# Performance work log

Hardware: AMD Instinct MI355X
Metric: run time of the kernel (lower is better)

## Reference

```python
import jax, jax.numpy as jnp
import numpy as np

B, C, H, W = 4, 256, 64, 64

def _conv1x1(x, w, b):
    # x: [B,C,H,W], w: [O,C] (1x1 conv kernel squeezed), b: [O]
    return jnp.einsum('bchw,oc->bohw', x, w) + b[None, :, None, None]

def setup_inputs() -> dict:
    key = jax.random.key(0)
    ks = jax.random.split(key, 9)
    s = 1.0 / np.sqrt(C)
    inp = {'x': jax.random.normal(ks[0], (B, C, H, W), dtype=jnp.float32)}
    for i, name in enumerate(['f', 'g', 'h', 'v']):
        inp['W' + name] = jax.random.uniform(ks[1 + 2 * i], (C, C), jnp.float32, -s, s)
        inp['b' + name] = jax.random.uniform(ks[2 + 2 * i], (C,), jnp.float32, -s, s)
    return inp

def reference(x, Wf, bf, Wg, bg, Wh, bh, Wv, bv):
    b, c, h, w = x.shape
    n = h * w
    f = _conv1x1(x, Wf, bf).reshape(b, c, n)  # [B,C,N]
    g = _conv1x1(x, Wg, bg).reshape(b, c, n)  # [B,C,N]
    hh = _conv1x1(x, Wh, bh).reshape(b, c, n)  # [B,C,N]
    fg = jnp.einsum('bci,bcj->bij', f, g)      # [B,N,N], no scaling (as in source)
    attn = jax.nn.softmax(fg, axis=1)          # softmax over dim=1 (first N axis)
    fgh = jnp.einsum('bci,bij->bcj', hh, attn) # [B,C,N]
    return _conv1x1(fgh.reshape(b, c, h, w), Wv, bv)
```

## Files before the change

kernel.cpp:

```cpp
#include <hip/hip_runtime.h>
#include <hip/hip_bf16.h>


typedef short short8 __attribute__((ext_vector_type(8)));
typedef float f32x4 __attribute__((ext_vector_type(4)));
typedef _Float16 f16x8 __attribute__((ext_vector_type(8)));
typedef unsigned short u16;

#define DEV static __device__ __forceinline__
#define MFMA(a, b, c)   __builtin_amdgcn_mfma_f32_16x16x32_bf16(a, b, c, 0, 0, 0)
#define MFMA16(a, b, c) __builtin_amdgcn_mfma_f32_16x16x32_f16(a, b, c, 0, 0, 0)

DEV u16 b16(float x) {
    __hip_bfloat16 h = __float2bfloat16(x);
    return *reinterpret_cast<u16*>(&h);
}
DEV float f16f(u16 u) {
    union { unsigned int ui; float f; } c;
    c.ui = ((unsigned int)u) << 16;
    return c.f;
}
DEV u16 h16(float x) {
    union { _Float16 h; u16 u; } c;
    c.h = (_Float16)x;
    return c.u;
}
DEV short8 ld8(const u16* p) { return *reinterpret_cast<const short8*>(p); }
DEV f16x8 ldh8(const u16* p) { return *reinterpret_cast<const f16x8*>(p); }

DEV void gload16(const void* g, void* l) {
    __builtin_amdgcn_global_load_lds(
        (const __attribute__((address_space(1))) unsigned int*)g,
        (__attribute__((address_space(3))) unsigned int*)l, 16, 0, 0);
}

constexpr size_t OFF_WFH = 0;
constexpr size_t OFF_WFL = 131072;
constexpr size_t OFF_WGH = 262144;
constexpr size_t OFF_WGL = 393216;
constexpr size_t OFF_WHB = 524288;
constexpr size_t OFF_WVB = 655360;
constexpr size_t OFF_ML  = 786432;
constexpr size_t OFF_F   = 1310720;
constexpr size_t OFF_G   = OFF_F + 8388608;
constexpr size_t OFF_H   = OFF_G + 8388608;
constexpr size_t OFF_XTH = OFF_H + 8388608;
constexpr size_t OFF_XTL = OFF_XTH + 8388608;
constexpr size_t OFF_OP  = OFF_XTH;
constexpr size_t OFF_OT  = OFF_F;

__global__ __launch_bounds__(256) void k_prep_w(
    const float* __restrict__ Wf, const float* __restrict__ Wg,
    const float* __restrict__ Wh, const float* __restrict__ Wv,
    u16* WFH, u16* WFL, u16* WGH, u16* WGL, u16* WHB, u16* WVB) {
    int i = blockIdx.x * 256 + threadIdx.x;
    float fv = Wf[i];
    u16 fh = b16(fv);
    WFH[i] = fh;
    WFL[i] = b16(fv - f16f(fh));
    float gv = Wg[i];
    u16 gh = b16(gv);
    WGH[i] = gh;
    WGL[i] = b16(gv - f16f(gh));
    WHB[i] = b16(Wh[i]);
    WVB[i] = h16(Wv[i]);
}

__global__ __launch_bounds__(256) void k_prep_x(const float* __restrict__ x, u16* XtH, u16* XtL) {
    __shared__ float lds[64][65];
    int bid = blockIdx.x;
    int b = bid >> 8, rem = bid & 255, ct = rem >> 6, nt = rem & 63;
    int tid = threadIdx.x;
    int tx = tid & 63, ty = tid >> 6;
    const float* src = x + ((size_t)(b * 256 + ct * 64)) * 4096 + nt * 64;
#pragma unroll
    for (int k = 0; k < 16; ++k) {
        int cl = ty * 16 + k;
        lds[cl][tx] = src[(size_t)cl * 4096 + tx];
    }
    __syncthreads();
    int nl = tid >> 2, cg = tid & 3;
    short8 h0, h1, l0, l1;
#pragma unroll
    for (int j = 0; j < 8; ++j) {
        float v = lds[cg * 16 + j][nl];
        u16 hb = b16(v);
        h0[j] = (short)hb;
        l0[j] = (short)b16(v - f16f(hb));
    }
#pragma unroll
    for (int j = 8; j < 16; ++j) {
        float v = lds[cg * 16 + j][nl];
        u16 hb = b16(v);
        h1[j - 8] = (short)hb;
        l1[j - 8] = (short)b16(v - f16f(hb));
    }
    size_t dst = ((size_t)(b * 4096 + nt * 64 + nl)) * 256 + ct * 64 + cg * 16;
    *reinterpret_cast<short8*>(XtH + dst) = h0;
    *reinterpret_cast<short8*>(XtH + dst + 8) = h1;
    *reinterpret_cast<short8*>(XtL + dst) = l0;
    *reinterpret_cast<short8*>(XtL + dst + 8) = l1;
}

__global__ __launch_bounds__(256) void k_conv_fg(
    const u16* __restrict__ XtH, const u16* __restrict__ XtL,
    const u16* __restrict__ WFH, const u16* __restrict__ WFL,
    const u16* __restrict__ WGH, const u16* __restrict__ WGL,
    const float* __restrict__ bf, const float* __restrict__ bg,
    u16* F, u16* G) {
    int bidm = blockIdx.x & 255, bido = blockIdx.x >> 8;
    int w = threadIdx.x >> 6, lane = threadIdx.x & 63, r = lane & 15, g = lane >> 4;
    int m0 = bidm * 64 + w * 16, o0 = bido * 64;
    f32x4 fa[4], ga[4];
#pragma unroll
    for (int i = 0; i < 4; ++i) { fa[i] = {0.f, 0.f, 0.f, 0.f}; ga[i] = {0.f, 0.f, 0.f, 0.f}; }
    const u16* arh = XtH + (size_t)(m0 + r) * 256;
    const u16* arl = XtL + (size_t)(m0 + r) * 256;
#pragma unroll
    for (int ks = 0; ks < 8; ++ks) {
        int k0 = ks * 32 + 8 * g;
        short8 ah = ld8(arh + k0);
        short8 al = ld8(arl + k0);
#pragma unroll
        for (int ot = 0; ot < 4; ++ot) {
            size_t wrow = (size_t)(o0 + ot * 16 + r) * 256 + k0;
            short8 wfh = ld8(WFH + wrow), wfl = ld8(WFL + wrow);
            short8 wgh = ld8(WGH + wrow), wgl = ld8(WGL + wrow);
            fa[ot] = MFMA(ah, wfh, fa[ot]);
            fa[ot] = MFMA(ah, wfl, fa[ot]);
            fa[ot] = MFMA(al, wfh, fa[ot]);
            ga[ot] = MFMA(ah, wgh, ga[ot]);
            ga[ot] = MFMA(ah, wgl, ga[ot]);
            ga[ot] = MFMA(al, wgh, ga[ot]);
        }
    }
#pragma unroll
    for (int ot = 0; ot < 4; ++ot) {
#pragma unroll
        for (int q = 0; q < 4; ++q) {
            int row = m0 + 4 * g + q;
            int col = o0 + ot * 16 + r;
            size_t idx = (size_t)row * 256 + col;
            F[idx] = h16(fa[ot][q] + bf[col]);
            G[idx] = h16(ga[ot][q] + bg[col]);
        }
    }
}

__global__ __launch_bounds__(256) void k_conv_h(
    const u16* __restrict__ WHB, const u16* __restrict__ XtH,
    const float* __restrict__ bh, u16* Hb) {
    int bidn = blockIdx.x & 255, bido = blockIdx.x >> 8;
    int w = threadIdx.x >> 6, lane = threadIdx.x & 63, r = lane & 15, g = lane >> 4;
    int o0 = bido * 64 + w * 16, n0 = bidn * 64;
    f32x4 acc[4];
#pragma unroll
    for (int i = 0; i < 4; ++i) acc[i] = {0.f, 0.f, 0.f, 0.f};
    const u16* arow = WHB + (size_t)(o0 + r) * 256;
#pragma unroll
    for (int ks = 0; ks < 8; ++ks) {
        int k0 = ks * 32 + 8 * g;
        short8 a = ld8(arow + k0);
#pragma unroll
        for (int ntl = 0; ntl < 4; ++ntl) {
            short8 bb = ld8(XtH + (size_t)(n0 + ntl * 16 + r) * 256 + k0);
            acc[ntl] = MFMA(a, bb, acc[ntl]);
        }
    }
#pragma unroll
    for (int ntl = 0; ntl < 4; ++ntl) {
#pragma unroll
        for (int q = 0; q < 4; ++q) {
            int o = o0 + 4 * g + q;
            int nf = n0 + ntl * 16 + r;
            int bb = nf >> 12, n = nf & 4095;
            Hb[((size_t)(bb * 256 + o)) * 4096 + n] = h16(acc[ntl][q] + bh[o]);
        }
    }
}

DEV float rmax16(float v) {
    v = fmaxf(v, __shfl_xor(v, 1));
    v = fmaxf(v, __shfl_xor(v, 2));
    v = fmaxf(v, __shfl_xor(v, 4));
    v = fmaxf(v, __shfl_xor(v, 8));
    return v;
}
DEV float rsum16(float v) {
    v += __shfl_xor(v, 1);
    v += __shfl_xor(v, 2);
    v += __shfl_xor(v, 4);
    v += __shfl_xor(v, 8);
    return v;
}

__global__ __launch_bounds__(256, 2) void k_attn(
    const u16* __restrict__ F, const u16* __restrict__ G,
    const u16* __restrict__ Hb, u16* __restrict__ OP, float* __restrict__ ML) {
    __shared__ u16 Klds[16384];
    __shared__ u16 Vlds[16384];

    int bid = blockIdx.x;
    int xcd = bid & 7;
    int b = xcd >> 1, ks = xcd & 1;
    int jt = bid >> 3;
    int tid = threadIdx.x;
    int w = tid >> 6, lane = tid & 63, r = lane & 15, g = lane >> 4;
    int j0 = jt * 64 + w * 16;
    const float L2E = 1.4426950408889634f;

    f16x8 Qf[8];
    {
        const u16* q = G + (size_t)(b * 4096 + j0 + r) * 256;
#pragma unroll
        for (int k = 0; k < 8; ++k) Qf[k] = ldh8(q + k * 32 + 8 * g);
    }
    f32x4 O[16];
#pragma unroll
    for (int i = 0; i < 16; ++i) O[i] = {0.f, 0.f, 0.f, 0.f};
    float m[4], l[4];
#pragma unroll
    for (int q = 0; q < 4; ++q) { m[q] = -1e30f; l[q] = 0.f; }

    const char* Fb  = (const char*)(F + (size_t)b * 4096 * 256);
    const char* Hbb = (const char*)(Hb + (size_t)b * 256 * 4096);
    char* Kl = (char*)Klds;
    char* Vl = (char*)Vlds;
    u16* Pw = Klds + w * 1280;

    for (int i0 = ks * 2048; i0 < ks * 2048 + 2048; i0 += 64) {
#pragma unroll
        for (int t = 0; t < 8; ++t) {
            int ti = w * 8 + t;
            int d = ti * 1024 + lane * 16;
            int row = d >> 9, cp = d & 511;
            gload16(Fb + (((size_t)(i0 + row)) << 9) + (size_t)(cp ^ ((row & 7) << 4)),
                    Kl + ti * 1024);
        }
#pragma unroll
        for (int t = 0; t < 8; ++t) {
            int ti = w * 8 + t;
            int d = ti * 1024 + lane * 16;
            int c = d >> 7, kb = d & 127;
            gload16(Hbb + (((size_t)c) << 13) + (size_t)(i0 * 2) + (size_t)(kb ^ ((c & 7) << 4)),
                    Vl + ti * 1024);
        }
        __syncthreads();

        f32x4 s[4];
#pragma unroll
        for (int it = 0; it < 4; ++it) s[it] = {0.f, 0.f, 0.f, 0.f};
#pragma unroll
        for (int it = 0; it < 4; ++it) {
            int row = it * 16 + r;
            const char* kr = Kl + row * 512;
            int sw = (row & 7) << 4;
#pragma unroll
            for (int k = 0; k < 8; ++k) {
                f16x8 kb = *reinterpret_cast<const f16x8*>(kr + ((k * 64 + 16 * g) ^ sw));
                s[it] = MFMA16(Qf[k], kb, s[it]);
            }
        }
        float corr[4];
#pragma unroll
        for (int q = 0; q < 4; ++q) {
            float v = fmaxf(fmaxf(s[0][q], s[1][q]), fmaxf(s[2][q], s[3][q]));
            v = rmax16(v);
            float mn = fmaxf(m[q], v);
            corr[q] = exp2f((m[q] - mn) * L2E);
            float rs = 0.f;
#pragma unroll
            for (int it = 0; it < 4; ++it) {
                float pv = exp2f((s[it][q] - mn) * L2E);
                s[it][q] = pv;
                rs += pv;
            }
            rs = rsum16(rs);
            l[q] = l[q] * corr[q] + rs;
            m[q] = mn;
        }
#pragma unroll
        for (int ct = 0; ct < 16; ++ct) {
            O[ct][0] *= corr[0];
            O[ct][1] *= corr[1];
            O[ct][2] *= corr[2];
            O[ct][3] *= corr[3];
        }
        __syncthreads();

#pragma unroll
        for (int it = 0; it < 4; ++it) {
#pragma unroll
            for (int q = 0; q < 4; ++q) Pw[(4 * g + q) * 72 + it * 16 + r] = h16(s[it][q]);
        }
        __asm__ volatile("s_waitcnt lgkmcnt(0)" ::: "memory");
        f16x8 pa0 = *reinterpret_cast<const f16x8*>((const char*)Pw + r * 144 + 16 * g);
        f16x8 pa1 = *reinterpret_cast<const f16x8*>((const char*)Pw + r * 144 + 64 + 16 * g);

#pragma unroll
        for (int ct = 0; ct < 16; ++ct) {
            int c = ct * 16 + r;
            const char* vr = Vl + c * 128;
            int sw = (c & 7) << 4;
            f16x8 v0 = *reinterpret_cast<const f16x8*>(vr + ((16 * g) ^ sw));
            f16x8 v1 = *reinterpret_cast<const f16x8*>(vr + ((64 + 16 * g) ^ sw));
            O[ct] = MFMA16(pa0, v0, O[ct]);
            O[ct] = MFMA16(pa1, v1, O[ct]);
        }
        __syncthreads();
    }
#pragma unroll
    for (int ct = 0; ct < 16; ++ct) {
#pragma unroll
        for (int q = 0; q < 4; ++q) {
            OP[((size_t)ks * 16384 + b * 4096 + j0 + 4 * g + q) * 256 + ct * 16 + r] = h16(O[ct][q]);
        }
    }
    if (r == 0) {
#pragma unroll
        for (int q = 0; q < 4; ++q) {
            size_t mi = ((size_t)ks * 16384 + b * 4096 + j0 + 4 * g + q) * 2;
            ML[mi] = m[q];
            ML[mi + 1] = l[q];
        }
    }
}

__global__ __launch_bounds__(256) void k_merge(
    const u16* __restrict__ OP, const float* __restrict__ ML, u16* __restrict__ OT) {
    int t = blockIdx.x * 256 + threadIdx.x;
    int m = t >> 5;
    int c0 = (t & 31) * 8;
    const float L2E = 1.4426950408889634f;
    float m0 = ML[(size_t)m * 2], l0 = ML[(size_t)m * 2 + 1];
    float m1 = ML[((size_t)16384 + m) * 2], l1 = ML[((size_t)16384 + m) * 2 + 1];
    float M = fmaxf(m0, m1);
    float w0 = exp2f((m0 - M) * L2E), w1 = exp2f((m1 - M) * L2E);
    float inv = 1.f / (w0 * l0 + w1 * l1);
    f16x8 v0 = ldh8(OP + (size_t)m * 256 + c0);
    f16x8 v1 = ldh8(OP + ((size_t)16384 + m) * 256 + c0);
    short8 outp;
#pragma unroll
    for (int j = 0; j < 8; ++j) outp[j] = (short)h16((w0 * (float)v0[j] + w1 * (float)v1[j]) * inv);
    *reinterpret_cast<short8*>(OT + (size_t)m * 256 + c0) = outp;
}

__global__ __launch_bounds__(256) void k_conv_out(
    const u16* __restrict__ WVB, const u16* __restrict__ OT,
    const float* __restrict__ bv, float* __restrict__ out) {
    int bidn = blockIdx.x & 255, bido = blockIdx.x >> 8;
    int w = threadIdx.x >> 6, lane = threadIdx.x & 63, r = lane & 15, g = lane >> 4;
    int o0 = bido * 64 + w * 16, n0 = bidn * 64;
    f32x4 acc[4];
#pragma unroll
    for (int i = 0; i < 4; ++i) acc[i] = {0.f, 0.f, 0.f, 0.f};
    const u16* arow = WVB + (size_t)(o0 + r) * 256;
#pragma unroll
    for (int ks = 0; ks < 8; ++ks) {
        int k0 = ks * 32 + 8 * g;
        f16x8 a = ldh8(arow + k0);
#pragma unroll
        for (int ntl = 0; ntl < 4; ++ntl) {
            f16x8 bb = ldh8(OT + (size_t)(n0 + ntl * 16 + r) * 256 + k0);
            acc[ntl] = MFMA16(a, bb, acc[ntl]);
        }
    }
#pragma unroll
    for (int ntl = 0; ntl < 4; ++ntl) {
#pragma unroll
        for (int q = 0; q < 4; ++q) {
            int o = o0 + 4 * g + q;
            int nf = n0 + ntl * 16 + r;
            int bb = nf >> 12, n = nf & 4095;
            out[((size_t)(bb * 256 + o)) * 4096 + n] = acc[ntl][q] + bv[o];
        }
    }
}

extern "C" void kernel_launch(void* const* d_in, const int* in_sizes, int n_in,
                              void* d_out, int out_size, void* d_ws, size_t ws_size,
                              hipStream_t stream) {
    const float* x  = (const float*)d_in[0];
    const float* Wf = (const float*)d_in[1];
    const float* bf = (const float*)d_in[2];
    const float* Wg = (const float*)d_in[3];
    const float* bg = (const float*)d_in[4];
    const float* Wh = (const float*)d_in[5];
    const float* bh = (const float*)d_in[6];
    const float* Wv = (const float*)d_in[7];
    const float* bv = (const float*)d_in[8];
    float* out = (float*)d_out;
    char* ws = (char*)d_ws;

    u16* WFH = (u16*)(ws + OFF_WFH);
    u16* WFL = (u16*)(ws + OFF_WFL);
    u16* WGH = (u16*)(ws + OFF_WGH);
    u16* WGL = (u16*)(ws + OFF_WGL);
    u16* WHB = (u16*)(ws + OFF_WHB);
    u16* WVB = (u16*)(ws + OFF_WVB);
    float* ML = (float*)(ws + OFF_ML);
    u16* F   = (u16*)(ws + OFF_F);
    u16* G   = (u16*)(ws + OFF_G);
    u16* H   = (u16*)(ws + OFF_H);
    u16* XTH = (u16*)(ws + OFF_XTH);
    u16* XTL = (u16*)(ws + OFF_XTL);
    u16* OP  = (u16*)(ws + OFF_OP);
    u16* OT  = (u16*)(ws + OFF_OT);

    k_prep_w<<<256, 256, 0, stream>>>(Wf, Wg, Wh, Wv, WFH, WFL, WGH, WGL, WHB, WVB);
    k_prep_x<<<1024, 256, 0, stream>>>(x, XTH, XTL);
    k_conv_fg<<<1024, 256, 0, stream>>>(XTH, XTL, WFH, WFL, WGH, WGL, bf, bg, F, G);
    k_conv_h<<<1024, 256, 0, stream>>>(WHB, XTH, bh, H);
    k_attn<<<512, 256, 0, stream>>>(F, G, H, OP, ML);
    k_merge<<<2048, 256, 0, stream>>>(OP, ML, OT);
    k_conv_out<<<1024, 256, 0, stream>>>(WVB, OT, bv, out);
}
```

Before: 254.9 us.

## Double-buffer attention K/V tiles, drop split-K merge, add lazy rescale

The attention kernel now walks all 4096 keys per block instead of splitting them across two blocks, which removes the partial-output/ML writes and the separate merge kernel. K and V tiles are double-buffered in LDS with global_load_lds prefetch of the next tile, and P gets its own LDS buffer, so one barrier per iteration replaces three. A lazy rescale skips the O correction when the running max grows by at most 8. The costs are half as many blocks (256), single-block occupancy from the larger LDS footprint, and a longer serial loop per block.

```diff
diff --git a/kernel.cpp b/kernel.cpp
--- a/kernel.cpp
+++ b/kernel.cpp
@@ -40,14 +40,12 @@
 constexpr size_t OFF_WGL = 393216;
 constexpr size_t OFF_WHB = 524288;
 constexpr size_t OFF_WVB = 655360;
-constexpr size_t OFF_ML  = 786432;
 constexpr size_t OFF_F   = 1310720;
 constexpr size_t OFF_G   = OFF_F + 8388608;
 constexpr size_t OFF_H   = OFF_G + 8388608;
 constexpr size_t OFF_XTH = OFF_H + 8388608;
 constexpr size_t OFF_XTL = OFF_XTH + 8388608;
-constexpr size_t OFF_OP  = OFF_XTH;
-constexpr size_t OFF_OT  = OFF_F;
+constexpr size_t OFF_OT  = OFF_XTH;
 
 __global__ __launch_bounds__(256) void k_prep_w(
     const float* __restrict__ Wf, const float* __restrict__ Wg,
@@ -194,19 +192,20 @@
     return v;
 }
 
-__global__ __launch_bounds__(256, 2) void k_attn(
+__global__ __launch_bounds__(256, 1) void k_attn(
     const u16* __restrict__ F, const u16* __restrict__ G,
-    const u16* __restrict__ Hb, u16* __restrict__ OP, float* __restrict__ ML) {
-    __shared__ u16 Klds[16384];
-    __shared__ u16 Vlds[16384];
+    const u16* __restrict__ Hb, u16* __restrict__ OT) {
+    __shared__ u16 Kd[2][16384];
+    __shared__ u16 Vd[2][16384];
+    __shared__ u16 Pd[4][1280];
 
     int bid = blockIdx.x;
     int xcd = bid & 7;
-    int b = xcd >> 1, ks = xcd & 1;
+    int b = xcd >> 1, half = xcd & 1;
     int jt = bid >> 3;
     int tid = threadIdx.x;
     int w = tid >> 6, lane = tid & 63, r = lane & 15, g = lane >> 4;
-    int j0 = jt * 64 + w * 16;
+    int j0 = half * 2048 + jt * 64 + w * 16;
     const float L2E = 1.4426950408889634f;
 
     f16x8 Qf[8];
@@ -224,74 +223,102 @@
 
     const char* Fb  = (const char*)(F + (size_t)b * 4096 * 256);
     const char* Hbb = (const char*)(Hb + (size_t)b * 256 * 4096);
-    char* Kl = (char*)Klds;
-    char* Vl = (char*)Vlds;
-    u16* Pw = Klds + w * 1280;
-
-    for (int i0 = ks * 2048; i0 < ks * 2048 + 2048; i0 += 64) {
-#pragma unroll
-        for (int t = 0; t < 8; ++t) {
-            int ti = w * 8 + t;
-            int d = ti * 1024 + lane * 16;
-            int row = d >> 9, cp = d & 511;
-            gload16(Fb + (((size_t)(i0 + row)) << 9) + (size_t)(cp ^ ((row & 7) << 4)),
-                    Kl + ti * 1024);
-        }
-#pragma unroll
-        for (int t = 0; t < 8; ++t) {
-            int ti = w * 8 + t;
-            int d = ti * 1024 + lane * 16;
-            int c = d >> 7, kb = d & 127;
-            gload16(Hbb + (((size_t)c) << 13) + (size_t)(i0 * 2) + (size_t)(kb ^ ((c & 7) << 4)),
-                    Vl + ti * 1024);
-        }
+    u16* Pw = Pd[w];
+
+    int koff[8], voff[8];
+#pragma unroll
+    for (int t = 0; t < 8; ++t) {
+        int d = (w * 8 + t) * 1024 + lane * 16;
+        koff[t] = d ^ (((d >> 9) & 7) << 4);
+        int c = d >> 7, kb = d & 127;
+        voff[t] = (c << 13) + (kb ^ (((c & 7)) << 4));
+    }
+
+#define STAGE(nxt, I0)                                                          \
+    do {                                                                        \
+        const char* kbase = Fb + (size_t)(I0) * 512;                            \
+        const char* vbase = Hbb + (size_t)(I0) * 2;                             \
+        char* kl = (char*)Kd[nxt];                                              \
+        char* vl = (char*)Vd[nxt];                                              \
+        _Pragma("unroll") for (int t = 0; t < 8; ++t)                           \
+            gload16(kbase + koff[t], kl + (w * 8 + t) * 1024);                  \
+        _Pragma("unroll") for (int t = 0; t < 8; ++t)                           \
+            gload16(vbase + voff[t], vl + (w * 8 + t) * 1024);                  \
+    } while (0)
+
+    STAGE(0, 0);
+
+    for (int it = 0; it < 64; ++it) {
+        int cur = it & 1;
         __syncthreads();
-
+        if (it + 1 < 64) STAGE(cur ^ 1, (it + 1) * 64);
+
+        const char* Kl = (const char*)Kd[cur];
+        const char* Vl = (const char*)Vd[cur];
         f32x4 s[4];
 #pragma unroll
-        for (int it = 0; it < 4; ++it) s[it] = {0.f, 0.f, 0.f, 0.f};
-#pragma unroll
-        for (int it = 0; it < 4; ++it) {
-            int row = it * 16 + r;
+        for (int it2 = 0; it2 < 4; ++it2) s[it2] = {0.f, 0.f, 0.f, 0.f};
+#pragma unroll
+        for (int it2 = 0; it2 < 4; ++it2) {
+            int row = it2 * 16 + r;
             const char* kr = Kl + row * 512;
             int sw = (row & 7) << 4;
 #pragma unroll
             for (int k = 0; k < 8; ++k) {
                 f16x8 kb = *reinterpret_cast<const f16x8*>(kr + ((k * 64 + 16 * g) ^ sw));
-                s[it] = MFMA16(Qf[k], kb, s[it]);
+                s[it2] = MFMA16(Qf[k], kb, s[it2]);
             }
         }
-        float corr[4];
+
+        float nm[4], grow = -1e30f;
 #pragma unroll
         for (int q = 0; q < 4; ++q) {
             float v = fmaxf(fmaxf(s[0][q], s[1][q]), fmaxf(s[2][q], s[3][q]));
             v = rmax16(v);
-            float mn = fmaxf(m[q], v);
-            corr[q] = exp2f((m[q] - mn) * L2E);
-            float rs = 0.f;
-#pragma unroll
-            for (int it = 0; it < 4; ++it) {
-                float pv = exp2f((s[it][q] - mn) * L2E);
-                s[it][q] = pv;
-                rs += pv;
+            nm[q] = v;
+            grow = fmaxf(grow, v - m[q]);
+        }
+        if (__all(grow <= 8.0f)) {
+#pragma unroll
+            for (int q = 0; q < 4; ++q) {
+                float rs = 0.f;
+#pragma unroll
+                for (int it2 = 0; it2 < 4; ++it2) {
+                    float pv = exp2f((s[it2][q] - m[q]) * L2E);
+                    s[it2][q] = pv;
+                    rs += pv;
+                }
+                l[q] += rsum16(rs);
             }
-            rs = rsum16(rs);
-            l[q] = l[q] * corr[q] + rs;
-            m[q] = mn;
-        }
-#pragma unroll
-        for (int ct = 0; ct < 16; ++ct) {
-            O[ct][0] *= corr[0];
-            O[ct][1] *= corr[1];
-            O[ct][2] *= corr[2];
-            O[ct][3] *= corr[3];
-        }
-        __syncthreads();
-
-#pragma unroll
-        for (int it = 0; it < 4; ++it) {
-#pragma unroll
-            for (int q = 0; q < 4; ++q) Pw[(4 * g + q) * 72 + it * 16 + r] = h16(s[it][q]);
+        } else {
+            float corr[4];
+#pragma unroll
+            for (int q = 0; q < 4; ++q) {
+                float mn = fmaxf(m[q], nm[q]);
+                corr[q] = exp2f((m[q] - mn) * L2E);
+                float rs = 0.f;
+#pragma unroll
+                for (int it2 = 0; it2 < 4; ++it2) {
+                    float pv = exp2f((s[it2][q] - mn) * L2E);
+                    s[it2][q] = pv;
+                    rs += pv;
+                }
+                l[q] = l[q] * corr[q] + rsum16(rs);
+                m[q] = mn;
+            }
+#pragma unroll
+            for (int ct = 0; ct < 16; ++ct) {
+                O[ct][0] *= corr[0];
+                O[ct][1] *= corr[1];
+                O[ct][2] *= corr[2];
+                O[ct][3] *= corr[3];
+            }
+        }
+
+#pragma unroll
+        for (int it2 = 0; it2 < 4; ++it2) {
+#pragma unroll
+            for (int q = 0; q < 4; ++q) Pw[(4 * g + q) * 72 + it2 * 16 + r] = h16(s[it2][q]);
         }
         __asm__ volatile("s_waitcnt lgkmcnt(0)" ::: "memory");
         f16x8 pa0 = *reinterpret_cast<const f16x8*>((const char*)Pw + r * 144 + 16 * g);
@@ -307,42 +334,19 @@
             O[ct] = MFMA16(pa0, v0, O[ct]);
             O[ct] = MFMA16(pa1, v1, O[ct]);
         }
-        __syncthreads();
-    }
+    }
+#undef STAGE
+
+    float inv[4];
+#pragma unroll
+    for (int q = 0; q < 4; ++q) inv[q] = 1.f / l[q];
 #pragma unroll
     for (int ct = 0; ct < 16; ++ct) {
 #pragma unroll
         for (int q = 0; q < 4; ++q) {
-            OP[((size_t)ks * 16384 + b * 4096 + j0 + 4 * g + q) * 256 + ct * 16 + r] = h16(O[ct][q]);
-        }
-    }
-    if (r == 0) {
-#pragma unroll
-        for (int q = 0; q < 4; ++q) {
-            size_t mi = ((size_t)ks * 16384 + b * 4096 + j0 + 4 * g + q) * 2;
-            ML[mi] = m[q];
-            ML[mi + 1] = l[q];
-        }
-    }
-}
-
-__global__ __launch_bounds__(256) void k_merge(
-    const u16* __restrict__ OP, const float* __restrict__ ML, u16* __restrict__ OT) {
-    int t = blockIdx.x * 256 + threadIdx.x;
-    int m = t >> 5;
-    int c0 = (t & 31) * 8;
-    const float L2E = 1.4426950408889634f;
-    float m0 = ML[(size_t)m * 2], l0 = ML[(size_t)m * 2 + 1];
-    float m1 = ML[((size_t)16384 + m) * 2], l1 = ML[((size_t)16384 + m) * 2 + 1];
-    float M = fmaxf(m0, m1);
-    float w0 = exp2f((m0 - M) * L2E), w1 = exp2f((m1 - M) * L2E);
-    float inv = 1.f / (w0 * l0 + w1 * l1);
-    f16x8 v0 = ldh8(OP + (size_t)m * 256 + c0);
-    f16x8 v1 = ldh8(OP + ((size_t)16384 + m) * 256 + c0);
-    short8 outp;
-#pragma unroll
-    for (int j = 0; j < 8; ++j) outp[j] = (short)h16((w0 * (float)v0[j] + w1 * (float)v1[j]) * inv);
-    *reinterpret_cast<short8*>(OT + (size_t)m * 256 + c0) = outp;
+            OT[(size_t)(b * 4096 + j0 + 4 * g + q) * 256 + ct * 16 + r] = h16(O[ct][q] * inv[q]);
+        }
+    }
 }
 
 __global__ __launch_bounds__(256) void k_conv_out(
@@ -398,20 +402,17 @@
     u16* WGL = (u16*)(ws + OFF_WGL);
     u16* WHB = (u16*)(ws + OFF_WHB);
     u16* WVB = (u16*)(ws + OFF_WVB);
-    float* ML = (float*)(ws + OFF_ML);
     u16* F   = (u16*)(ws + OFF_F);
     u16* G   = (u16*)(ws + OFF_G);
     u16* H   = (u16*)(ws + OFF_H);
     u16* XTH = (u16*)(ws + OFF_XTH);
     u16* XTL = (u16*)(ws + OFF_XTL);
-    u16* OP  = (u16*)(ws + OFF_OP);
     u16* OT  = (u16*)(ws + OFF_OT);
 
     k_prep_w<<<256, 256, 0, stream>>>(Wf, Wg, Wh, Wv, WFH, WFL, WGH, WGL, WHB, WVB);
     k_prep_x<<<1024, 256, 0, stream>>>(x, XTH, XTL);
     k_conv_fg<<<1024, 256, 0, stream>>>(XTH, XTL, WFH, WFL, WGH, WGL, bf, bg, F, G);
     k_conv_h<<<1024, 256, 0, stream>>>(WHB, XTH, bh, H);
-    k_attn<<<512, 256, 0, stream>>>(F, G, H, OP, ML);
-    k_merge<<<2048, 256, 0, stream>>>(OP, ML, OT);
+    k_attn<<<256, 256, 0, stream>>>(F, G, H, OT);
     k_conv_out<<<1024, 256, 0, stream>>>(WVB, OT, bv, out);
 }
```

After: 305.3 us. +19.8%, slower.

## Double-buffer K/V tiles in attention with lazy softmax rescaling and prio hints

Applied to the files above, without the earlier changes.

The attention kernel now double-buffers 32-key K and V tiles in shared memory, issuing the next tile's loads before computing on the current one. This is meant to hide global-load latency and removes one barrier per iteration. It also skips the running-max update and accumulator rescale when the max grows by at most 8, raises wave priority around MFMA blocks, and normalizes partial outputs before the merge. The cost is twice as many loop iterations on smaller tiles, and the lazy max risks fp16 overflow of the exp terms if the threshold is too loose.

```diff
diff --git a/kernel.cpp b/kernel.cpp
--- a/kernel.cpp
+++ b/kernel.cpp
@@ -6,6 +6,7 @@
 typedef float f32x4 __attribute__((ext_vector_type(4)));
 typedef _Float16 f16x8 __attribute__((ext_vector_type(8)));
 typedef unsigned short u16;
+typedef unsigned int u32;
 
 #define DEV static __device__ __forceinline__
 #define MFMA(a, b, c)   __builtin_amdgcn_mfma_f32_16x16x32_bf16(a, b, c, 0, 0, 0)
@@ -197,16 +198,16 @@
 __global__ __launch_bounds__(256, 2) void k_attn(
     const u16* __restrict__ F, const u16* __restrict__ G,
     const u16* __restrict__ Hb, u16* __restrict__ OP, float* __restrict__ ML) {
-    __shared__ u16 Klds[16384];
-    __shared__ u16 Vlds[16384];
+    __shared__ u16 Kd[2][8192];
+    __shared__ u16 Vd[2][8192];
+    __shared__ u16 Pd[4][1152];
 
     int bid = blockIdx.x;
-    int xcd = bid & 7;
+    int xcd = bid & 7, idx = bid >> 3;
     int b = xcd >> 1, ks = xcd & 1;
-    int jt = bid >> 3;
     int tid = threadIdx.x;
     int w = tid >> 6, lane = tid & 63, r = lane & 15, g = lane >> 4;
-    int j0 = jt * 64 + w * 16;
+    int j0 = idx * 64 + w * 16;
     const float L2E = 1.4426950408889634f;
 
     f16x8 Qf[8];
@@ -224,96 +225,131 @@
 
     const char* Fb  = (const char*)(F + (size_t)b * 4096 * 256);
     const char* Hbb = (const char*)(Hb + (size_t)b * 256 * 4096);
-    char* Kl = (char*)Klds;
-    char* Vl = (char*)Vlds;
-    u16* Pw = Klds + w * 1280;
-
-    for (int i0 = ks * 2048; i0 < ks * 2048 + 2048; i0 += 64) {
-#pragma unroll
-        for (int t = 0; t < 8; ++t) {
-            int ti = w * 8 + t;
-            int d = ti * 1024 + lane * 16;
-            int row = d >> 9, cp = d & 511;
-            gload16(Fb + (((size_t)(i0 + row)) << 9) + (size_t)(cp ^ ((row & 7) << 4)),
-                    Kl + ti * 1024);
-        }
-#pragma unroll
-        for (int t = 0; t < 8; ++t) {
-            int ti = w * 8 + t;
-            int d = ti * 1024 + lane * 16;
-            int c = d >> 7, kb = d & 127;
-            gload16(Hbb + (((size_t)c) << 13) + (size_t)(i0 * 2) + (size_t)(kb ^ ((c & 7) << 4)),
-                    Vl + ti * 1024);
-        }
-        __syncthreads();
-
-        f32x4 s[4];
-#pragma unroll
-        for (int it = 0; it < 4; ++it) s[it] = {0.f, 0.f, 0.f, 0.f};
-#pragma unroll
-        for (int it = 0; it < 4; ++it) {
-            int row = it * 16 + r;
+    u16* Pw = Pd[w];
+
+    int ksrc[4], vsrc[4];
+#pragma unroll
+    for (int t = 0; t < 4; ++t) {
+        int d = (w * 4 + t) * 1024 + lane * 16;
+        int row = d >> 9, col = d & 511;
+        ksrc[t] = row * 512 + (col ^ ((row & 7) << 4));
+        int r128 = d >> 7, wn = d & 127;
+        int wp = wn ^ ((r128 & 7) << 4);
+        vsrc[t] = ((r128 * 2 + (wp >> 6)) << 13) + (wp & 63);
+    }
+
+#define STAGE(bufn, I0)                                                         \
+    do {                                                                        \
+        const char* kb_ = Fb + (size_t)(I0) * 512;                              \
+        const char* vb_ = Hbb + (size_t)(I0) * 2;                               \
+        char* kl = (char*)Kd[bufn];                                             \
+        char* vl = (char*)Vd[bufn];                                             \
+        _Pragma("unroll") for (int t = 0; t < 4; ++t)                           \
+            gload16(kb_ + ksrc[t], kl + (w * 4 + t) * 1024);                    \
+        _Pragma("unroll") for (int t = 0; t < 4; ++t)                           \
+            gload16(vb_ + vsrc[t], vl + (w * 4 + t) * 1024);                    \
+    } while (0)
+
+    int i0beg = ks * 2048;
+    STAGE(0, i0beg);
+    __syncthreads();
+
+    for (int it = 0; it < 64; ++it) {
+        int cur = it & 1;
+        if (it + 1 < 64) STAGE(cur ^ 1, i0beg + (it + 1) * 32);
+
+        const char* Kl = (const char*)Kd[cur];
+        const char* Vl = (const char*)Vd[cur];
+
+        f32x4 s[2];
+        s[0] = {0.f, 0.f, 0.f, 0.f};
+        s[1] = {0.f, 0.f, 0.f, 0.f};
+        __builtin_amdgcn_s_setprio(1);
+#pragma unroll
+        for (int it2 = 0; it2 < 2; ++it2) {
+            int row = it2 * 16 + r;
             const char* kr = Kl + row * 512;
             int sw = (row & 7) << 4;
 #pragma unroll
             for (int k = 0; k < 8; ++k) {
                 f16x8 kb = *reinterpret_cast<const f16x8*>(kr + ((k * 64 + 16 * g) ^ sw));
-                s[it] = MFMA16(Qf[k], kb, s[it]);
+                s[it2] = MFMA16(Qf[k], kb, s[it2]);
             }
         }
-        float corr[4];
-#pragma unroll
-        for (int q = 0; q < 4; ++q) {
-            float v = fmaxf(fmaxf(s[0][q], s[1][q]), fmaxf(s[2][q], s[3][q]));
+        __builtin_amdgcn_s_setprio(0);
+
+        float nm[4], grow = -1e30f;
+#pragma unroll
+        for (int q = 0; q < 4; ++q) {
+            float v = fmaxf(s[0][q], s[1][q]);
             v = rmax16(v);
-            float mn = fmaxf(m[q], v);
-            corr[q] = exp2f((m[q] - mn) * L2E);
-            float rs = 0.f;
-#pragma unroll
-            for (int it = 0; it < 4; ++it) {
-                float pv = exp2f((s[it][q] - mn) * L2E);
-                s[it][q] = pv;
-                rs += pv;
+            nm[q] = v;
+            grow = fmaxf(grow, v - m[q]);
+        }
+        if (__all(grow <= 8.0f)) {
+#pragma unroll
+            for (int q = 0; q < 4; ++q) {
+                float p0 = exp2f((s[0][q] - m[q]) * L2E);
+                float p1 = exp2f((s[1][q] - m[q]) * L2E);
+                s[0][q] = p0;
+                s[1][q] = p1;
+                l[q] += rsum16(p0 + p1);
             }
-            rs = rsum16(rs);
-            l[q] = l[q] * corr[q] + rs;
-            m[q] = mn;
-        }
-#pragma unroll
-        for (int ct = 0; ct < 16; ++ct) {
-            O[ct][0] *= corr[0];
-            O[ct][1] *= corr[1];
-            O[ct][2] *= corr[2];
-            O[ct][3] *= corr[3];
-        }
-        __syncthreads();
-
-#pragma unroll
-        for (int it = 0; it < 4; ++it) {
-#pragma unroll
-            for (int q = 0; q < 4; ++q) Pw[(4 * g + q) * 72 + it * 16 + r] = h16(s[it][q]);
+        } else {
+            float corr[4];
+#pragma unroll
+            for (int q = 0; q < 4; ++q) {
+                float mn = fmaxf(m[q], nm[q]);
+                corr[q] = exp2f((m[q] - mn) * L2E);
+                float p0 = exp2f((s[0][q] - mn) * L2E);
+                float p1 = exp2f((s[1][q] - mn) * L2E);
+                s[0][q] = p0;
+                s[1][q] = p1;
+                l[q] = l[q] * corr[q] + rsum16(p0 + p1);
+                m[q] = mn;
+            }
+#pragma unroll
+            for (int ct = 0; ct < 16; ++ct) {
+                O[ct][0] *= corr[0];
+                O[ct][1] *= corr[1];
+                O[ct][2] *= corr[2];
+                O[ct][3] *= corr[3];
+            }
+        }
+
+#pragma unroll
+        for (int it2 = 0; it2 < 2; ++it2) {
+#pragma unroll
+            for (int q = 0; q < 4; ++q) Pw[(4 * g + q) * 72 + it2 * 16 + r] = h16(s[it2][q]);
         }
         __asm__ volatile("s_waitcnt lgkmcnt(0)" ::: "memory");
-        f16x8 pa0 = *reinterpret_cast<const f16x8*>((const char*)Pw + r * 144 + 16 * g);
-        f16x8 pa1 = *reinterpret_cast<const f16x8*>((const char*)Pw + r * 144 + 64 + 16 * g);
-
+        f16x8 pa = *reinterpret_cast<const f16x8*>((const char*)Pw + r * 144 + 16 * g);
+
+        __builtin_amdgcn_s_setprio(1);
 #pragma unroll
         for (int ct = 0; ct < 16; ++ct) {
             int c = ct * 16 + r;
-            const char* vr = Vl + c * 128;
-            int sw = (c & 7) << 4;
-            f16x8 v0 = *reinterpret_cast<const f16x8*>(vr + ((16 * g) ^ sw));
-            f16x8 v1 = *reinterpret_cast<const f16x8*>(vr + ((64 + 16 * g) ^ sw));
-            O[ct] = MFMA16(pa0, v0, O[ct]);
-            O[ct] = MFMA16(pa1, v1, O[ct]);
-        }
+            const char* vr = Vl + (c >> 1) * 128;
+            int swv = ((c >> 1) & 7) << 4;
+            int cb = (c & 1) * 64;
+            f16x8 vb = *reinterpret_cast<const f16x8*>(vr + ((16 * g + cb) ^ swv));
+            O[ct] = MFMA16(pa, vb, O[ct]);
+        }
+        __builtin_amdgcn_s_setprio(0);
+
         __syncthreads();
     }
+#undef STAGE
+
+    float inv[4];
+#pragma unroll
+    for (int q = 0; q < 4; ++q) inv[q] = 1.f / l[q];
 #pragma unroll
     for (int ct = 0; ct < 16; ++ct) {
 #pragma unroll
         for (int q = 0; q < 4; ++q) {
-            OP[((size_t)ks * 16384 + b * 4096 + j0 + 4 * g + q) * 256 + ct * 16 + r] = h16(O[ct][q]);
+            OP[((size_t)ks * 16384 + b * 4096 + j0 + 4 * g + q) * 256 + ct * 16 + r] =
+                h16(O[ct][q] * inv[q]);
         }
     }
     if (r == 0) {
@@ -335,13 +371,15 @@
     float m0 = ML[(size_t)m * 2], l0 = ML[(size_t)m * 2 + 1];
     float m1 = ML[((size_t)16384 + m) * 2], l1 = ML[((size_t)16384 + m) * 2 + 1];
     float M = fmaxf(m0, m1);
-    float w0 = exp2f((m0 - M) * L2E), w1 = exp2f((m1 - M) * L2E);
-    float inv = 1.f / (w0 * l0 + w1 * l1);
+    float wl0 = exp2f((m0 - M) * L2E) * l0;
+    float wl1 = exp2f((m1 - M) * L2E) * l1;
+    float inv = 1.f / (wl0 + wl1);
     f16x8 v0 = ldh8(OP + (size_t)m * 256 + c0);
     f16x8 v1 = ldh8(OP + ((size_t)16384 + m) * 256 + c0);
     short8 outp;
 #pragma unroll
-    for (int j = 0; j < 8; ++j) outp[j] = (short)h16((w0 * (float)v0[j] + w1 * (float)v1[j]) * inv);
+    for (int j = 0; j < 8; ++j)
+        outp[j] = (short)h16((wl0 * (float)v0[j] + wl1 * (float)v1[j]) * inv);
     *reinterpret_cast<short8*>(OT + (size_t)m * 256 + c0) = outp;
 }
 
```

After: 288.2 us. 13.1% more time.
